# Kernel optimization log

Measured on AMD Instinct MI355X. Metric: run time of the kernel, lower is better.

The kernel has to match this reference:

```python
import jax, jax.numpy as jnp
import numpy as np

N = 20000   # nodes
E = 40000   # edges
B = 1000    # graphs
F = 32      # num_features
D = 64      # dim


def setup_inputs() -> dict:
    key = jax.random.key(0)
    ks = jax.random.split(key, 16)
    def g(k, shape, scale=0.05):
        return jax.random.normal(k, shape, jnp.float32) * scale
    return dict(
        x=jax.random.normal(ks[0], (N, F), jnp.float32),
        edge_attr=jax.random.uniform(ks[1], (E, 5), jnp.float32),
        edge_index=jax.random.randint(ks[2], (2, E), 0, N),
        batch=jnp.sort(jax.random.randint(ks[3], (N,), 0, B)),
        W0=g(ks[4], (D, F)), b0=jnp.zeros((D,), jnp.float32),
        We1=g(ks[5], (128, 5)), be1=jnp.zeros((128,), jnp.float32),
        We2=g(ks[6], (D * D, 128), 0.01), be2=jnp.zeros((D * D,), jnp.float32),
        b_conv=jnp.zeros((D,), jnp.float32),
        W_ih=g(ks[7], (3 * D, D)), W_hh=g(ks[8], (3 * D, D)),
        b_ih=jnp.zeros((3 * D,), jnp.float32), b_hh=jnp.zeros((3 * D,), jnp.float32),
        W_ihl=g(ks[9], (4 * D, 2 * D)), W_hhl=g(ks[10], (4 * D, D)),
        b_ihl=jnp.zeros((4 * D,), jnp.float32), b_hhl=jnp.zeros((4 * D,), jnp.float32),
        W1=g(ks[11], (D, 2 * D)), b1=jnp.zeros((D,), jnp.float32),
        W2=g(ks[12], (1, D)), b2=jnp.zeros((1,), jnp.float32),
    )


def reference(x, edge_attr, edge_index, batch, W0, b0, We1, be1, We2, be2,
              b_conv, W_ih, W_hh, b_ih, b_hh, W_ihl, W_hhl, b_ihl, b_hhl,
              W1, b1, W2, b2):
    src, dst = edge_index[0], edge_index[1]
    # lin0 + relu
    out = jax.nn.relu(x @ W0.T + b0)            # [N, D]
    h = out                                     # GRU hidden
    # edge-conditioned weights (identical each iteration in the original)
    We = jax.nn.relu(edge_attr @ We1.T + be1) @ We2.T + be2
    We = We.reshape(E, D, D)                    # [E, in, out]
    deg = jnp.maximum(jax.ops.segment_sum(jnp.ones((E,), out.dtype), dst, N), 1.0)[:, None]
    for _ in range(3):
        msg = jnp.einsum('ei,eio->eo', out[src], We)          # [E, D]
        agg = jax.ops.segment_sum(msg, dst, num_segments=N) / deg
        m = jax.nn.relu(agg + b_conv)
        # GRU cell (gate order r, z, n as in torch)
        gi = m @ W_ih.T + b_ih
        gh = h @ W_hh.T + b_hh
        ir, iz, inn = jnp.split(gi, 3, -1)
        hr, hz, hn = jnp.split(gh, 3, -1)
        r = jax.nn.sigmoid(ir + hr)
        z = jax.nn.sigmoid(iz + hz)
        n = jnp.tanh(inn + r * hn)
        h = (1.0 - z) * n + z * h
        out = h
    # Set2Set pooling (3 processing steps), LSTM gate order i, f, g, o
    q_star = jnp.zeros((B, 2 * D), out.dtype)
    hl = jnp.zeros((B, D), out.dtype)
    cl = jnp.zeros((B, D), out.dtype)
    for _ in range(3):
        gates = q_star @ W_ihl.T + b_ihl + hl @ W_hhl.T + b_hhl
        i_, f_, g_, o_ = jnp.split(gates, 4, -1)
        cl = jax.nn.sigmoid(f_) * cl + jax.nn.sigmoid(i_) * jnp.tanh(g_)
        hl = jax.nn.sigmoid(o_) * jnp.tanh(cl)
        q = hl                                               # [B, D]
        e = jnp.sum(out * q[batch], -1)                      # [N]
        emax = jax.ops.segment_max(e, batch, num_segments=B)
        a = jnp.exp(e - emax[batch])
        a = a / jax.ops.segment_sum(a, batch, num_segments=B)[batch]
        r_ = jax.ops.segment_sum(a[:, None] * out, batch, num_segments=B)
        q_star = jnp.concatenate([q, r_], -1)                # [B, 2D]
    y = jax.nn.relu(q_star @ W1.T + b1)
    pred = (y @ W2.T + b2).reshape(-1)                       # [B]
    return pred
```

## Files before the change

### kernel.cpp

```cpp
#include <hip/hip_runtime.h>

#define NN 20000
#define NE 40000
#define NGR 1000
#define KH 2
#define WTF_BIAS 524288

typedef unsigned short u16;
typedef u16 u16x8 __attribute__((ext_vector_type(8)));
typedef __bf16 bf16x8 __attribute__((ext_vector_type(8)));
typedef float f32x4 __attribute__((ext_vector_type(4)));

union U8 { u16x8 u; bf16x8 b; };

__device__ __forceinline__ u16 f2bf(float f) {
    union { float f; unsigned u; } v; v.f = f;
    unsigned r = v.u + 0x7FFF + ((v.u >> 16) & 1);
    return (u16)(r >> 16);
}
__device__ __forceinline__ float bf2f(u16 h) {
    union { unsigned u; float f; } v; v.u = ((unsigned)h) << 16;
    return v.f;
}
__device__ __forceinline__ float sigmoidf(float x) { return 1.f / (1.f + __expf(-x)); }

__global__ __launch_bounds__(256) void k_cnt(const int* __restrict__ ei, int* __restrict__ cnt)
{
    for (int e = blockIdx.x * 256 + threadIdx.x; e < NE; e += gridDim.x * 256)
        atomicAdd(&cnt[ei[NE + e]], 1);
}

__global__ __launch_bounds__(1024) void k_scan(const int* __restrict__ cnt,
                                               int* __restrict__ rowptr)
{
    __shared__ int ps[1024];
    int t = threadIdx.x;
    int base = t * 20;
    int loc[20];
    int s = 0;
#pragma unroll
    for (int i = 0; i < 20; ++i) {
        int idx = base + i;
        loc[i] = s;
        s += (idx < NN) ? cnt[idx] : 0;
    }
    ps[t] = s;
    __syncthreads();
    for (int off = 1; off < 1024; off <<= 1) {
        int v = (t >= off) ? ps[t - off] : 0;
        __syncthreads();
        ps[t] += v;
        __syncthreads();
    }
    int ex = (t > 0) ? ps[t - 1] : 0;
#pragma unroll
    for (int i = 0; i < 20; ++i) {
        int idx = base + i;
        if (idx < NN) rowptr[idx] = ex + loc[i];
    }
    if (t == 1023) rowptr[NN] = ps[1023];
}

__global__ __launch_bounds__(256) void k_scatter(const int* __restrict__ ei,
    const int* __restrict__ rowptr, int* __restrict__ cur,
    int* __restrict__ epos, int* __restrict__ srcs)
{
    for (int e = blockIdx.x * 256 + threadIdx.x; e < NE; e += gridDim.x * 256) {
        int d = ei[NE + e];
        int pos = rowptr[d] + atomicAdd(&cur[d], 1);
        epos[e] = pos;
        srcs[pos] = ei[e];
    }
}

__global__ __launch_bounds__(256) void k_pre(
    const float* __restrict__ x, const float* __restrict__ ea,
    const int* __restrict__ batch, const int* __restrict__ epos,
    const float* __restrict__ W0, const float* __restrict__ b0,
    const float* __restrict__ We1, const float* __restrict__ be1,
    const float* __restrict__ We2, const float* __restrict__ be2,
    const float* __restrict__ W_ih, const float* __restrict__ W_hh,
    const float* __restrict__ W_ihl, const float* __restrict__ W_hhl,
    const float* __restrict__ W1,
    float* __restrict__ h, u16* __restrict__ outb, u16* __restrict__ h1,
    u16* __restrict__ WtF, int* __restrict__ gstart, int* __restrict__ gend,
    u16* __restrict__ WgF,
    float* __restrict__ WTihl, float* __restrict__ WThhl, float* __restrict__ WT1)
{
    const int b = blockIdx.x;
    const int t = threadIdx.x;

    if (b < 64) {
        for (int idx = b * 256 + t; idx < 90112; idx += 64 * 256) {
            int i = idx;
            if (i < 32768) {
                int j = i & 7, lane = (i >> 3) & 63;
                int nt = (i >> 9) & 15, ks = i >> 13;
                int o = nt * 16 + (lane & 15);
                int k = ks * 32 + (lane >> 4) * 8 + j;
                float v;
                if (o < 128)      v = (k < 64) ? W_ih[o * 64 + k] : W_hh[o * 64 + k - 64];
                else if (o < 192) v = (k < 64) ? W_ih[o * 64 + k] : 0.f;
                else              v = (k >= 64) ? W_hh[(o - 64) * 64 + k - 64] : 0.f;
                WgF[i] = f2bf(v);
                continue;
            }
            i -= 32768;
            if (i < 32768) { WTihl[i] = W_ihl[(i % 256) * 128 + i / 256]; continue; }
            i -= 32768;
            if (i < 16384) { WThhl[i] = W_hhl[(i % 256) * 64 + i / 256]; continue; }
            i -= 16384;
            WT1[i] = W1[(i % 64) * 128 + i / 64];
        }
        return;
    }
    if (b < 320) {
        int wv = (b - 64) * 4 + (t >> 6);
        int lane = t & 63;
        float w0r[32];
#pragma unroll
        for (int f = 0; f < 32; ++f) w0r[f] = W0[lane * 32 + f];
        float b0v = b0[lane];
        for (int n = wv; n < NN; n += 1024) {
            float xv = (lane < 32) ? x[n * 32 + lane] : 0.f;
            float acc = b0v;
#pragma unroll
            for (int f = 0; f < 32; ++f) acc += __shfl(xv, f, 64) * w0r[f];
            float rv = fmaxf(acc, 0.f);
            h[n * 64 + lane] = rv;
            outb[n * 64 + lane] = f2bf(rv);
        }
        return;
    }
    if (b < 832) {
        for (int idx = (b - 320) * 256 + t; idx < NE * 128; idx += 512 * 256) {
            int e = idx >> 7, k = idx & 127;
            float acc = be1[k];
#pragma unroll
            for (int j = 0; j < 5; ++j)
                acc += ea[e * 5 + j] * We1[k * 5 + j];
            h1[(size_t)epos[e] * 128 + k] = f2bf(fmaxf(acc, 0.f));
        }
        return;
    }
    if (b < 960) {
        for (int idx = (b - 832) * 256 + t; idx < WTF_BIAS + 4096; idx += 128 * 256) {
            float v;
            if (idx < WTF_BIAS) {
                int j = idx & 7, lane = (idx >> 3) & 63;
                int nt = (idx >> 9) & 3, s4 = (idx >> 11) & 3, ch = idx >> 13;
                int o = nt * 16 + (lane & 15);
                int k = s4 * 32 + (lane >> 4) * 8 + j;
                v = We2[(size_t)(ch * 64 + o) * 128 + k];
            } else {
                int bx = idx - WTF_BIAS;
                int j = bx & 7, lane = (bx >> 3) & 63;
                int nt = (bx >> 9) & 3, sb = bx >> 11;
                int o = nt * 16 + (lane & 15);
                int i = sb * 32 + (lane >> 4) * 8 + j;
                v = be2[i * 64 + o];
            }
            WtF[idx] = f2bf(v);
        }
        return;
    }
    {
        for (int idx = (b - 960) * 256 + t; idx < NN; idx += 32 * 256) {
            int bg = batch[idx];
            if (idx == 0 || batch[idx - 1] != bg) gstart[bg] = idx;
            if (idx == NN - 1 || batch[idx + 1] != bg) gend[bg] = idx + 1;
        }
    }
}

__global__ __launch_bounds__(256, 2) void k_msg(
    const u16* __restrict__ outb, const u16* __restrict__ h1,
    const u16* __restrict__ WtF, const int* __restrict__ srcs,
    u16* __restrict__ pbuf)
{
    __shared__ __align__(8) u16 svT[64 * 260];
    const int t = threadIdx.x;
    const int eb0 = blockIdx.x * 256;
    const int kh = blockIdx.y;

#pragma unroll
    for (int r = 0; r < 8; ++r) {
        int cid = t + 256 * r;
        int row = cid >> 3, c8 = cid & 7;
        int e = eb0 + row;
        u16x8 v = {};
        if (e < NE) { int s = srcs[e]; v = *(const u16x8*)(outb + (size_t)s * 64 + c8 * 8); }
#pragma unroll
        for (int j = 0; j < 8; ++j)
            svT[(c8 * 8 + j) * 260 + row] = v[j];
    }

    const int lane = t & 63, w = t >> 6, r16 = lane & 15, q = lane >> 4;
    const int w64 = w * 64;

    u16x8 h1r[4][4];
#pragma unroll
    for (int sub = 0; sub < 4; ++sub) {
        int e = eb0 + w64 + sub * 16 + r16;
        if (e >= NE) e = NE - 1;
        const u16* hp = h1 + (size_t)e * 128 + q * 8;
#pragma unroll
        for (int s4 = 0; s4 < 4; ++s4)
            h1r[sub][s4] = *(const u16x8*)(hp + s4 * 32);
    }

    f32x4 acc[4][4];
    f32x4 P[4][4];
    const f32x4 z4 = {0.f, 0.f, 0.f, 0.f};
#pragma unroll
    for (int sub = 0; sub < 4; ++sub)
#pragma unroll
        for (int nt = 0; nt < 4; ++nt) acc[sub][nt] = z4;

    U8 bA[4], bB[4];
    auto LD = [&](U8* dst, int ch, int s4) {
        const u16* p = WtF + (size_t)ch * 8192 + s4 * 2048 + lane * 8;
#pragma unroll
        for (int nt = 0; nt < 4; ++nt)
            dst[nt].u = *(const u16x8*)(p + nt * 512);
    };
    auto MF0 = [&](U8* bv, int s4) {
#pragma unroll
        for (int sub = 0; sub < 4; ++sub) {
            U8 a; a.u = h1r[sub][s4];
#pragma unroll
            for (int nt = 0; nt < 4; ++nt)
                P[sub][nt] = __builtin_amdgcn_mfma_f32_16x16x32_bf16(
                    a.b, bv[nt].b, z4, 0, 0, 0);
        }
    };
    auto MF = [&](U8* bv, int s4) {
#pragma unroll
        for (int sub = 0; sub < 4; ++sub) {
            U8 a; a.u = h1r[sub][s4];
#pragma unroll
            for (int nt = 0; nt < 4; ++nt)
                P[sub][nt] = __builtin_amdgcn_mfma_f32_16x16x32_bf16(
                    a.b, bv[nt].b, P[sub][nt], 0, 0, 0);
        }
    };

    __syncthreads();
    LD(bA, kh * 32, 0);

#pragma unroll 1
    for (int cc = 0; cc < 32; ++cc) {
        const int ch = kh * 32 + cc;
        LD(bB, ch, 1);  MF0(bA, 0);
        LD(bA, ch, 2);  MF (bB, 1);
        LD(bB, ch, 3);  MF (bA, 2);
        if (cc < 31) LD(bA, ch + 1, 0);
        MF(bB, 3);

#pragma unroll
        for (int sub = 0; sub < 4; ++sub) {
            int mb = w64 + sub * 16 + q * 4;
            uint2 rv = *(const uint2*)&svT[ch * 260 + mb];
            union { unsigned u; float f; } c0, c1, c2, c3;
            c0.u = rv.x << 16; c1.u = rv.x & 0xffff0000u;
            c2.u = rv.y << 16; c3.u = rv.y & 0xffff0000u;
#pragma unroll
            for (int nt = 0; nt < 4; ++nt) {
                acc[sub][nt][0] += c0.f * P[sub][nt][0];
                acc[sub][nt][1] += c1.f * P[sub][nt][1];
                acc[sub][nt][2] += c2.f * P[sub][nt][2];
                acc[sub][nt][3] += c3.f * P[sub][nt][3];
            }
        }
    }

    if (kh == KH - 1) {
        U8 bvb[2][4];
#pragma unroll
        for (int sb = 0; sb < 2; ++sb)
#pragma unroll
            for (int nt = 0; nt < 4; ++nt)
                bvb[sb][nt].u = *(const u16x8*)(WtF + WTF_BIAS + ((sb * 4 + nt) * 64 + lane) * 8);
#pragma unroll
        for (int sub = 0; sub < 4; ++sub) {
            int m = w64 + sub * 16 + r16;
#pragma unroll
            for (int sb = 0; sb < 2; ++sb) {
                U8 a;
#pragma unroll
                for (int j = 0; j < 8; ++j)
                    a.u[j] = svT[(sb * 32 + q * 8 + j) * 260 + m];
#pragma unroll
                for (int nt = 0; nt < 4; ++nt)
                    acc[sub][nt] = __builtin_amdgcn_mfma_f32_16x16x32_bf16(
                        a.b, bvb[sb][nt].b, acc[sub][nt], 0, 0, 0);
            }
        }
    }

#pragma unroll
    for (int sub = 0; sub < 4; ++sub) {
#pragma unroll
        for (int r = 0; r < 4; ++r) {
            int e = eb0 + w64 + sub * 16 + q * 4 + r;
            if (e >= NE) continue;
            u16* pp = pbuf + (size_t)e * (KH * 64) + kh * 64 + r16;
#pragma unroll
            for (int nt = 0; nt < 4; ++nt)
                pp[nt * 16] = f2bf(acc[sub][nt][r]);
        }
    }
}

__global__ __launch_bounds__(256) void k_gru(float* __restrict__ h, u16* __restrict__ outb,
    const u16* __restrict__ pbuf, const int* __restrict__ rowptr,
    const float* __restrict__ b_conv, const u16* __restrict__ WgF,
    const float* __restrict__ b_ih, const float* __restrict__ b_hh)
{
    __shared__ __align__(16) u16 zA[64 * 132];
    __shared__ float hS[64 * 65];
    const int t = threadIdx.x;
    const int lane = t & 63, w = t >> 6, r16 = lane & 15, q = lane >> 4;
    const int n0 = blockIdx.x * 64;
    const int w16 = w * 16;
    float bcv = b_conv[lane];

#pragma unroll 1
    for (int p = 0; p < 16; ++p) {
        int n = n0 + w16 + p;
        float m = 0.f, hvv = 0.f;
        if (n < NN) {
            int rs = rowptr[n], re = rowptr[n + 1];
            float v = 0.f;
            const u16* pb = pbuf + (size_t)rs * (KH * 64);
            for (int j = rs; j < re; ++j) {
                v += bf2f(pb[lane]) + bf2f(pb[64 + lane]);
                pb += KH * 64;
            }
            m = fmaxf(v / fmaxf((float)(re - rs), 1.f) + bcv, 0.f);
            hvv = h[n * 64 + lane];
        }
        zA[(w16 + p) * 132 + lane] = f2bf(m);
        zA[(w16 + p) * 132 + 64 + lane] = f2bf(hvv);
        hS[(w16 + p) * 65 + lane] = hvv;
    }

    u16x8 afr[4];
#pragma unroll
    for (int ks = 0; ks < 4; ++ks)
        afr[ks] = *(const u16x8*)&zA[(w16 + r16) * 132 + ks * 32 + q * 8];

    f32x4 acc[16];
    const f32x4 z4 = {0.f, 0.f, 0.f, 0.f};
#pragma unroll
    for (int nt = 0; nt < 16; ++nt) acc[nt] = z4;

    U8 bA[4], bB[4];
    auto LDB = [&](U8* dst, int nt) {
#pragma unroll
        for (int ks = 0; ks < 4; ++ks)
            dst[ks].u = *(const u16x8*)(WgF + ((ks * 16 + nt) * 64 + lane) * 8);
    };
    LDB(bA, 0);
#pragma unroll
    for (int nt = 0; nt < 16; ++nt) {
        U8* cur = (nt & 1) ? bB : bA;
        U8* nxt = (nt & 1) ? bA : bB;
        if (nt < 15) LDB(nxt, nt + 1);
        f32x4 c = acc[nt];
#pragma unroll
        for (int ks = 0; ks < 4; ++ks) {
            U8 a; a.u = afr[ks];
            c = __builtin_amdgcn_mfma_f32_16x16x32_bf16(a.b, cur[ks].b, c, 0, 0, 0);
        }
        acc[nt] = c;
    }

#pragma unroll
    for (int reg = 0; reg < 4; ++reg) {
        int nl = w16 + q * 4 + reg;
        int n = n0 + nl;
        if (n >= NN) continue;
#pragma unroll
        for (int dd = 0; dd < 4; ++dd) {
            int d = dd * 16 + r16;
            float rv = acc[dd][reg]      + b_ih[d]       + b_hh[d];
            float zv = acc[4 + dd][reg]  + b_ih[64 + d]  + b_hh[64 + d];
            float iv = acc[8 + dd][reg]  + b_ih[128 + d];
            float hg = acc[12 + dd][reg] + b_hh[128 + d];
            float rr = sigmoidf(rv), zz = sigmoidf(zv);
            float nn = tanhf(iv + rr * hg);
            float hold = hS[nl * 65 + d];
            float hnew = (1.f - zz) * nn + zz * hold;
            h[n * 64 + d] = hnew;
            outb[n * 64 + d] = f2bf(hnew);
        }
    }
}

__global__ __launch_bounds__(256) void k_s2s(const float* __restrict__ h,
    const int* __restrict__ gstart, const int* __restrict__ gend,
    const float* __restrict__ WTihl, const float* __restrict__ WThhl,
    const float* __restrict__ b_ihl, const float* __restrict__ b_hhl,
    const float* __restrict__ WT1, const float* __restrict__ b1,
    const float* __restrict__ W2, const float* __restrict__ b2,
    float* __restrict__ outp)
{
    __shared__ float qs[128];
    __shared__ float hlL[64], clL[64];
    __shared__ float gt[256];
    __shared__ float sm[4], sl[4], sr[4][64];
    const int g = blockIdx.x;
    const int t = threadIdx.x, w = t >> 6, lane = t & 63;
    const int s = gstart[g], e = gend[g];

    if (t < 128) qs[t] = 0.f;
    if (t < 64) { hlL[t] = 0.f; clL[t] = 0.f; }
    __syncthreads();

    for (int step = 0; step < 3; ++step) {
        float ga = b_ihl[t] + b_hhl[t];
#pragma unroll 4
        for (int j = 0; j < 128; ++j)
            ga += qs[j] * WTihl[j * 256 + t];
#pragma unroll 4
        for (int j = 0; j < 64; ++j)
            ga += hlL[j] * WThhl[j * 256 + t];
        gt[t] = ga;
        __syncthreads();
        if (t < 64) {
            float cv = sigmoidf(gt[64 + t]) * clL[t] + sigmoidf(gt[t]) * tanhf(gt[128 + t]);
            float hn = sigmoidf(gt[192 + t]) * tanhf(cv);
            clL[t] = cv; hlL[t] = hn; qs[t] = hn;
        }
        __syncthreads();
        float qv = hlL[lane];
        float M = -3.4e38f, l = 0.f, r = 0.f;
        for (int n = s + w; n < e; n += 4) {
            float hvv = h[n * 64 + lane];
            float p = hvv * qv;
#pragma unroll
            for (int off = 32; off > 0; off >>= 1) p += __shfl_xor(p, off, 64);
            if (p > M) {
                float sc = __expf(M - p);
                l = l * sc + 1.f;
                r = r * sc + hvv;
                M = p;
            } else {
                float pe = __expf(p - M);
                l += pe;
                r += pe * hvv;
            }
        }
        if (lane == 0) { sm[w] = M; sl[w] = l; }
        sr[w][lane] = r;
        __syncthreads();
        if (w == 0) {
            float Mg = fmaxf(fmaxf(sm[0], sm[1]), fmaxf(sm[2], sm[3]));
            float lg = 0.f, rg = 0.f;
#pragma unroll
            for (int wp = 0; wp < 4; ++wp) {
                float sc = __expf(sm[wp] - Mg);
                lg += sl[wp] * sc;
                rg += sr[wp][lane] * sc;
            }
            float inv = (lg > 0.f) ? 1.f / lg : 0.f;
            qs[64 + lane] = rg * inv;
        }
        __syncthreads();
    }
    float acc = 0.f;
#pragma unroll 4
    for (int j = w * 32; j < w * 32 + 32; ++j)
        acc += qs[j] * WT1[j * 64 + lane];
    sr[w][lane] = acc;
    __syncthreads();
    if (w == 0) {
        float y = sr[0][lane] + sr[1][lane] + sr[2][lane] + sr[3][lane] + b1[lane];
        float pr = fmaxf(y, 0.f) * W2[lane];
#pragma unroll
        for (int off = 32; off > 0; off >>= 1) pr += __shfl_xor(pr, off, 64);
        if (lane == 0) outp[g] = pr + b2[0];
    }
}

extern "C" void kernel_launch(void* const* d_in, const int* in_sizes, int n_in,
                              void* d_out, int out_size, void* d_ws, size_t ws_size,
                              hipStream_t stream)
{
    const float* x      = (const float*)d_in[0];
    const float* ea     = (const float*)d_in[1];
    const int*   ei     = (const int*)d_in[2];
    const int*   batch  = (const int*)d_in[3];
    const float* W0     = (const float*)d_in[4];
    const float* b0     = (const float*)d_in[5];
    const float* We1    = (const float*)d_in[6];
    const float* be1    = (const float*)d_in[7];
    const float* We2    = (const float*)d_in[8];
    const float* be2    = (const float*)d_in[9];
    const float* b_conv = (const float*)d_in[10];
    const float* W_ih   = (const float*)d_in[11];
    const float* W_hh   = (const float*)d_in[12];
    const float* b_ih   = (const float*)d_in[13];
    const float* b_hh   = (const float*)d_in[14];
    const float* W_ihl  = (const float*)d_in[15];
    const float* W_hhl  = (const float*)d_in[16];
    const float* b_ihl  = (const float*)d_in[17];
    const float* b_hhl  = (const float*)d_in[18];
    const float* W1     = (const float*)d_in[19];
    const float* b1     = (const float*)d_in[20];
    const float* W2     = (const float*)d_in[21];
    const float* b2     = (const float*)d_in[22];
    float* outp = (float*)d_out;

    char* ws = (char*)d_ws;
    size_t off = 0;
    auto alloc = [&](size_t bytes) -> char* {
        char* p = ws + off;
        off += (bytes + 255) & ~(size_t)255;
        return p;
    };
    u16*   h1     = (u16*)  alloc((size_t)NE * 128 * 2);
    u16*   WtF    = (u16*)  alloc((WTF_BIAS + 4096) * 2);
    u16*   outb   = (u16*)  alloc((size_t)NN * 64 * 2);
    float* h      = (float*)alloc((size_t)NN * 64 * 4);
    u16*   pbuf   = (u16*)  alloc((size_t)NE * KH * 64 * 2);
    int*   rowptr = (int*)  alloc((NN + 1) * 4);
    int*   epos   = (int*)  alloc(NE * 4);
    int*   srcs   = (int*)  alloc(NE * 4);
    int*   cnt    = (int*)  alloc(NN * 4);
    int*   cur    = (int*)  alloc(NN * 4);
    int*   gstart = (int*)  alloc(NGR * 4);
    int*   gend   = (int*)  alloc(NGR * 4);
    u16*   WgF    = (u16*)  alloc(32768 * 2);
    float* WTihl  = (float*)alloc(32768 * 4);
    float* WThhl  = (float*)alloc(16384 * 4);
    float* WT1    = (float*)alloc(8192 * 4);
    if (off > ws_size) return;

    size_t zspan = (size_t)((char*)(gend + NGR) - (char*)cnt);
    hipMemsetAsync(cnt, 0, zspan, stream);

    k_cnt<<<64, 256, 0, stream>>>(ei, cnt);
    k_scan<<<1, 1024, 0, stream>>>(cnt, rowptr);
    k_scatter<<<64, 256, 0, stream>>>(ei, rowptr, cur, epos, srcs);
    k_pre<<<992, 256, 0, stream>>>(x, ea, batch, epos, W0, b0, We1, be1, We2, be2,
                                   W_ih, W_hh, W_ihl, W_hhl, W1,
                                   h, outb, h1, WtF, gstart, gend,
                                   WgF, WTihl, WThhl, WT1);

    dim3 mgrid((NE + 255) / 256, KH, 1);
    for (int it = 0; it < 3; ++it) {
        k_msg<<<mgrid, 256, 0, stream>>>(outb, h1, WtF, srcs, pbuf);
        k_gru<<<313, 256, 0, stream>>>(h, outb, pbuf, rowptr, b_conv,
                                       WgF, b_ih, b_hh);
    }
    k_s2s<<<NGR, 256, 0, stream>>>(h, gstart, gend, WTihl, WThhl, b_ihl, b_hhl,
                                   WT1, b1, W2, b2, outp);
}
```

Before: 450.4 us.

## Split k_msg output columns across grid z and load whole weight chunks per step

Adds a third grid dimension that splits the 64 output columns of the edge-message kernel into two halves, so each block holds half the accumulators and partial products. The weight chunk for all four K-slices is now loaded at once into a double buffer, and the loop processes two chunks per iteration. This doubles the block count and lowers register pressure, which may improve occupancy and latency hiding. The cost is that the source-row gather into shared memory and the h1 loads are duplicated across the two column halves.

Result: no change. 442.1 us (-1.9%).

```diff
diff --git a/kernel.cpp b/kernel.cpp
--- a/kernel.cpp
+++ b/kernel.cpp
@@ -182,6 +182,7 @@
     const int t = threadIdx.x;
     const int eb0 = blockIdx.x * 256;
     const int kh = blockIdx.y;
+    const int ohc = (int)blockIdx.z * 2;
 
 #pragma unroll
     for (int r = 0; r < 8; ++r) {
@@ -209,54 +210,34 @@
             h1r[sub][s4] = *(const u16x8*)(hp + s4 * 32);
     }
 
-    f32x4 acc[4][4];
-    f32x4 P[4][4];
+    f32x4 acc[4][2];
     const f32x4 z4 = {0.f, 0.f, 0.f, 0.f};
 #pragma unroll
     for (int sub = 0; sub < 4; ++sub)
 #pragma unroll
-        for (int nt = 0; nt < 4; ++nt) acc[sub][nt] = z4;
-
-    U8 bA[4], bB[4];
-    auto LD = [&](U8* dst, int ch, int s4) {
-        const u16* p = WtF + (size_t)ch * 8192 + s4 * 2048 + lane * 8;
-#pragma unroll
-        for (int nt = 0; nt < 4; ++nt)
-            dst[nt].u = *(const u16x8*)(p + nt * 512);
+        for (int nt = 0; nt < 2; ++nt) acc[sub][nt] = z4;
+
+    U8 bufA[8], bufB[8];
+    auto LDC = [&](U8 (&dst)[8], int ch) {
+        const u16* p = WtF + (size_t)ch * 8192 + ohc * 512 + lane * 8;
+#pragma unroll
+        for (int s4 = 0; s4 < 4; ++s4)
+#pragma unroll
+            for (int nt = 0; nt < 2; ++nt)
+                dst[s4 * 2 + nt].u = *(const u16x8*)(p + s4 * 2048 + nt * 512);
     };
-    auto MF0 = [&](U8* bv, int s4) {
-#pragma unroll
-        for (int sub = 0; sub < 4; ++sub) {
-            U8 a; a.u = h1r[sub][s4];
-#pragma unroll
-            for (int nt = 0; nt < 4; ++nt)
-                P[sub][nt] = __builtin_amdgcn_mfma_f32_16x16x32_bf16(
-                    a.b, bv[nt].b, z4, 0, 0, 0);
-        }
-    };
-    auto MF = [&](U8* bv, int s4) {
-#pragma unroll
-        for (int sub = 0; sub < 4; ++sub) {
-            U8 a; a.u = h1r[sub][s4];
-#pragma unroll
-            for (int nt = 0; nt < 4; ++nt)
-                P[sub][nt] = __builtin_amdgcn_mfma_f32_16x16x32_bf16(
-                    a.b, bv[nt].b, P[sub][nt], 0, 0, 0);
-        }
-    };
-
-    __syncthreads();
-    LD(bA, kh * 32, 0);
-
-#pragma unroll 1
-    for (int cc = 0; cc < 32; ++cc) {
-        const int ch = kh * 32 + cc;
-        LD(bB, ch, 1);  MF0(bA, 0);
-        LD(bA, ch, 2);  MF (bB, 1);
-        LD(bB, ch, 3);  MF (bA, 2);
-        if (cc < 31) LD(bA, ch + 1, 0);
-        MF(bB, 3);
-
+    auto STEP = [&](U8 (&bv)[8], int ch) {
+        f32x4 P[4][2];
+#pragma unroll
+        for (int s4 = 0; s4 < 4; ++s4)
+#pragma unroll
+            for (int sub = 0; sub < 4; ++sub) {
+                U8 a; a.u = h1r[sub][s4];
+#pragma unroll
+                for (int nt = 0; nt < 2; ++nt)
+                    P[sub][nt] = __builtin_amdgcn_mfma_f32_16x16x32_bf16(
+                        a.b, bv[s4 * 2 + nt].b, (s4 == 0) ? z4 : P[sub][nt], 0, 0, 0);
+            }
 #pragma unroll
         for (int sub = 0; sub < 4; ++sub) {
             int mb = w64 + sub * 16 + q * 4;
@@ -265,22 +246,35 @@
             c0.u = rv.x << 16; c1.u = rv.x & 0xffff0000u;
             c2.u = rv.y << 16; c3.u = rv.y & 0xffff0000u;
 #pragma unroll
-            for (int nt = 0; nt < 4; ++nt) {
+            for (int nt = 0; nt < 2; ++nt) {
                 acc[sub][nt][0] += c0.f * P[sub][nt][0];
                 acc[sub][nt][1] += c1.f * P[sub][nt][1];
                 acc[sub][nt][2] += c2.f * P[sub][nt][2];
                 acc[sub][nt][3] += c3.f * P[sub][nt][3];
             }
         }
+    };
+
+    LDC(bufA, kh * 32);
+    __syncthreads();
+
+#pragma unroll 1
+    for (int cc = 0; cc < 32; cc += 2) {
+        const int ch = kh * 32 + cc;
+        LDC(bufB, ch + 1);
+        STEP(bufA, ch);
+        if (cc < 30) LDC(bufA, ch + 2);
+        STEP(bufB, ch + 1);
     }
 
     if (kh == KH - 1) {
-        U8 bvb[2][4];
+        U8 bvb[2][2];
 #pragma unroll
         for (int sb = 0; sb < 2; ++sb)
 #pragma unroll
-            for (int nt = 0; nt < 4; ++nt)
-                bvb[sb][nt].u = *(const u16x8*)(WtF + WTF_BIAS + ((sb * 4 + nt) * 64 + lane) * 8);
+            for (int nt = 0; nt < 2; ++nt)
+                bvb[sb][nt].u = *(const u16x8*)(WtF + WTF_BIAS +
+                                                ((sb * 4 + ohc + nt) * 64 + lane) * 8);
 #pragma unroll
         for (int sub = 0; sub < 4; ++sub) {
             int m = w64 + sub * 16 + r16;
@@ -291,7 +285,7 @@
                 for (int j = 0; j < 8; ++j)
                     a.u[j] = svT[(sb * 32 + q * 8 + j) * 260 + m];
 #pragma unroll
-                for (int nt = 0; nt < 4; ++nt)
+                for (int nt = 0; nt < 2; ++nt)
                     acc[sub][nt] = __builtin_amdgcn_mfma_f32_16x16x32_bf16(
                         a.b, bvb[sb][nt].b, acc[sub][nt], 0, 0, 0);
             }
@@ -306,8 +300,8 @@
             if (e >= NE) continue;
             u16* pp = pbuf + (size_t)e * (KH * 64) + kh * 64 + r16;
 #pragma unroll
-            for (int nt = 0; nt < 4; ++nt)
-                pp[nt * 16] = f2bf(acc[sub][nt][r]);
+            for (int nt = 0; nt < 2; ++nt)
+                pp[(ohc + nt) * 16] = f2bf(acc[sub][nt][r]);
         }
     }
 }
@@ -549,7 +543,7 @@
                                    h, outb, h1, WtF, gstart, gend,
                                    WgF, WTihl, WThhl, WT1);
 
-    dim3 mgrid((NE + 255) / 256, KH, 1);
+    dim3 mgrid((NE + 255) / 256, KH, 2);
     for (int it = 0; it < 3; ++it) {
         k_msg<<<mgrid, 256, 0, stream>>>(outb, h1, WtF, srcs, pbuf);
         k_gru<<<313, 256, 0, stream>>>(h, outb, pbuf, rowptr, b_conv,
```
